# Performance work log

Hardware: AMD Instinct MI355X
Metric: run time of the kernel (lower is better)

Reference implementation:

```python
import jax, jax.numpy as jnp
import numpy as np

N = 10000        # nodes
E = 320000       # edges (before self-loops)
G = 100          # graphs in batch
HEADS = 2
OUT = 125        # per-head out channels
NEG_SLOPE = 0.2  # PyG GATConv default leaky_relu slope


def setup_inputs() -> dict:
    key = jax.random.key(0)
    k = lambda i: jax.random.fold_in(key, i)
    rn = lambda i, shape, s=0.1: jax.random.normal(k(i), shape, jnp.float32) * s
    inp = {
        "x": jax.random.normal(k(0), (N, 336), jnp.float32),
        "edge_index": jax.random.randint(k(1), (2, E), 0, N, jnp.int32),
        "batch": jnp.sort(jax.random.randint(k(2), (N,), 0, G, jnp.int32)),
    }
    conv_in = [336, 250, 250, 250]
    for i, din in enumerate(conv_in, start=1):
        base = 10 * i
        inp[f"W{i}"] = rn(base, (din, HEADS * OUT))
        inp[f"asrc{i}"] = rn(base + 1, (HEADS, OUT))
        inp[f"adst{i}"] = rn(base + 2, (HEADS, OUT))
        inp[f"b{i}"] = jnp.zeros((HEADS * OUT,), jnp.float32)
    lin_dims = [(250, 200), (200, 100), (100, 100), (100, 29)]
    for i, (din, dout) in enumerate(lin_dims, start=1):
        inp[f"lw{i}"] = rn(100 + i, (din, dout))
        inp[f"lb{i}"] = jnp.zeros((dout,), jnp.float32)
    return inp


def gat_conv(x, src, dst, W, asrc, adst, b):
    # PyG GATConv (v1), concat heads, self-loops already in (src, dst).
    n = x.shape[0]
    h = (x @ W).reshape(n, HEADS, OUT)                    # [N,H,C]
    e_src = jnp.einsum('nhc,hc->nh', h, asrc)             # a_src . h_j
    e_dst = jnp.einsum('nhc,hc->nh', h, adst)             # a_dst . h_i
    e = jax.nn.leaky_relu(e_src[src] + e_dst[dst], NEG_SLOPE)  # [Etot,H]
    m = jax.ops.segment_max(e, dst, num_segments=n)       # segment softmax over incoming edges
    e = jnp.exp(e - m[dst])
    denom = jax.ops.segment_sum(e, dst, num_segments=n)
    alpha = e / (denom[dst] + 1e-16)                      # [Etot,H]
    out = jax.ops.segment_sum(alpha[:, :, None] * h[src], dst, num_segments=n)
    return out.reshape(n, HEADS * OUT) + b


def reference(x, edge_index, batch,
              W1, asrc1, adst1, b1, W2, asrc2, adst2, b2,
              W3, asrc3, adst3, b3, W4, asrc4, adst4, b4,
              lw1, lb1, lw2, lb2, lw3, lb3, lw4, lb4):
    n = x.shape[0]
    loop = jnp.arange(n, dtype=edge_index.dtype)
    src = jnp.concatenate([edge_index[0], loop])          # add_self_loops=True
    dst = jnp.concatenate([edge_index[1], loop])

    h = jax.nn.relu(gat_conv(x, src, dst, W1, asrc1, adst1, b1))
    h = jax.nn.relu(gat_conv(h, src, dst, W2, asrc2, adst2, b2))
    h = jax.nn.relu(gat_conv(h, src, dst, W3, asrc3, adst3, b3))
    h = jax.nn.relu(gat_conv(h, src, dst, W4, asrc4, adst4, b4))

    # global_mean_pool over graph ids
    sums = jax.ops.segment_sum(h, batch, num_segments=G)
    cnts = jax.ops.segment_sum(jnp.ones((n, 1), h.dtype), batch, num_segments=G)
    g = sums / jnp.maximum(cnts, 1.0)                     # [G,250]

    g = jax.nn.relu(g @ lw1 + lb1)
    g = jax.nn.relu(g @ lw2 + lb2)
    g = jax.nn.relu(g @ lw3 + lb3)
    return g @ lw4 + lb4                                  # [G,29]
```

## Files before the change

kernel.cpp:

```cpp
#include <hip/hip_runtime.h>
#include <hip/hip_bf16.h>

#define NNODES 10000
#define NEDGES 320000
#define ETOT   (NEDGES + NNODES)
#define NGRAPH 100
#define CH     250
#define HOUT   125
#define MPAD   10048
#define NTILE  157
#define KP0    352
#define KP1    256
#define HPAD   256
#define ECAP   128
#define DCAPW  128
#define APAD   264

typedef __attribute__((ext_vector_type(8))) short bf16x8;
typedef __attribute__((ext_vector_type(4))) float f32x4;

static __device__ __forceinline__ float bflo(unsigned int u){
  union{ unsigned int i; float f; } v; v.i = u << 16; return v.f;
}
static __device__ __forceinline__ float bfhi(unsigned int u){
  union{ unsigned int i; float f; } v; v.i = u & 0xffff0000u; return v.f;
}
static __device__ __forceinline__ unsigned short f2bfbits(float f){
  __hip_bfloat16 b = __float2bfloat16(f);
  union{ __hip_bfloat16 b; unsigned short s; } v; v.b = b; return v.s;
}

struct Args {
  const float* x; const int* eidx; const int* batch;
  const float *W0,*W1,*W2,*W3;
  __hip_bfloat16 *Abf0, *Wt0, *Wt1, *Wt2, *Wt3;
  int *cursor; unsigned short* bucket; int *gstart;
};

__global__ void k_pre(Args a){
  int gtid = blockIdx.x * blockDim.x + threadIdx.x;
  int gstr = gridDim.x * blockDim.x;
  for (int e = gtid; e < ETOT; e += gstr){
    int dst, src;
    if (e < NEDGES){ src = a.eidx[e]; dst = a.eidx[NEDGES + e]; }
    else           { src = e - NEDGES; dst = src; }
    int pos = atomicAdd(&a.cursor[dst], 1);
    if (pos < ECAP) a.bucket[(size_t)dst * ECAP + pos] = (unsigned short)src;
  }
  for (int n = gtid; n < NNODES; n += gstr){
    int b1 = a.batch[n];
    int b0 = (n == 0) ? -1 : a.batch[n-1];
    for (int b = b0 + 1; b <= b1; ++b) a.gstart[b] = n;
    if (n == NNODES - 1){
      for (int b = b1 + 1; b <= NGRAPH; ++b) a.gstart[b] = NNODES;
    }
  }
  for (int j = gtid; j < NNODES * 84; j += gstr){
    int r = j / 84, c4 = (j - r * 84) * 4;
    float4 v = *(const float4*)(a.x + (size_t)r * 336 + c4);
    ushort4 o;
    o.x = f2bfbits(v.x); o.y = f2bfbits(v.y); o.z = f2bfbits(v.z); o.w = f2bfbits(v.w);
    *(ushort4*)(a.Abf0 + (size_t)r * KP0 + c4) = o;
  }
  const int T0 = 16 * KP0 * 16;
  const int T1 = 16 * KP1 * 16;
  int tot = T0 + 3*T1;
  for (int i = gtid; i < tot; i += gstr){
    const float* W; __hip_bfloat16* Wt; int K, Kp, li;
    if (i < T0)             { W = a.W0; Wt = a.Wt0; K = 336; Kp = KP0; li = i; }
    else if (i < T0 +   T1) { W = a.W1; Wt = a.Wt1; K = CH;  Kp = KP1; li = i - T0; }
    else if (i < T0 + 2*T1) { W = a.W2; Wt = a.Wt2; K = CH;  Kp = KP1; li = i - T0 - T1; }
    else                    { W = a.W3; Wt = a.Wt3; K = CH;  Kp = KP1; li = i - T0 - 2*T1; }
    int KC = Kp >> 5;
    int nt = li / (Kp * 16);
    int rem = li % (Kp * 16);
    int k = rem / 16;
    int n = rem % 16;
    int col = nt * 16 + n;
    float v = (k < K && col < CH) ? W[(size_t)k * CH + col] : 0.f;
    Wt[(((size_t)nt * KC + (k >> 5)) * 16 + n) * 32 + (k & 31)] = __float2bfloat16(v);
  }
}

__global__ __launch_bounds__(256) void k_gemm(
    const __hip_bfloat16* __restrict__ A, const __hip_bfloat16* __restrict__ Wt,
    __hip_bfloat16* __restrict__ Cb, const float* __restrict__ asrc,
    const float* __restrict__ adst, float* __restrict__ esrc, float* __restrict__ edst,
    int Kp){
  int wv = threadIdx.x >> 6, lane = threadIdx.x & 63;
  int n16 = lane & 15, q = lane >> 4;
  int KC = Kp >> 5;
  int rowbase = blockIdx.x * 64 + wv * 16;
  int bn = blockIdx.y * 64;
  int nt0 = bn >> 4;
  const __hip_bfloat16* ap = A  + (size_t)(rowbase + n16) * Kp + q * 8;
  const __hip_bfloat16* bp = Wt + ((size_t)nt0 * KC * 16 + n16) * 32 + q * 8;
  f32x4 ac0 = {0.f,0.f,0.f,0.f}, ac1 = ac0, ac2 = ac0, ac3 = ac0;
  for (int kc = 0; kc < KC; ++kc){
    bf16x8 a  = *(const bf16x8*)(ap + (size_t)kc * 32);
    bf16x8 b0 = *(const bf16x8*)(bp + ((size_t)0 * KC + kc) * 512);
    bf16x8 b1 = *(const bf16x8*)(bp + ((size_t)1 * KC + kc) * 512);
    bf16x8 b2 = *(const bf16x8*)(bp + ((size_t)2 * KC + kc) * 512);
    bf16x8 b3 = *(const bf16x8*)(bp + ((size_t)3 * KC + kc) * 512);
    ac0 = __builtin_amdgcn_mfma_f32_16x16x32_bf16(a, b0, ac0, 0, 0, 0);
    ac1 = __builtin_amdgcn_mfma_f32_16x16x32_bf16(a, b1, ac1, 0, 0, 0);
    ac2 = __builtin_amdgcn_mfma_f32_16x16x32_bf16(a, b2, ac2, 0, 0, 0);
    ac3 = __builtin_amdgcn_mfma_f32_16x16x32_bf16(a, b3, ac3, 0, 0, 0);
  }
  float es0[4] = {}, es1[4] = {}, ed0a[4] = {}, ed1a[4] = {};
  #define SCORE_T(AC, T) { \
    int col = bn + (T)*16 + n16; \
    bool ok = col < CH; \
    float av = ok ? asrc[col] : 0.f; \
    float dv = ok ? adst[col] : 0.f; \
    bool hh = col >= HOUT; \
    float av0 = hh ? 0.f : av, av1 = hh ? av : 0.f; \
    float dv0 = hh ? 0.f : dv, dv1 = hh ? dv : 0.f; \
    _Pragma("unroll") \
    for (int r = 0; r < 4; ++r){ \
      es0[r] += AC[r]*av0; es1[r] += AC[r]*av1; \
      ed0a[r] += AC[r]*dv0; ed1a[r] += AC[r]*dv1; } }
  SCORE_T(ac0, 0) SCORE_T(ac1, 1) SCORE_T(ac2, 2) SCORE_T(ac3, 3)
  #undef SCORE_T
  #pragma unroll
  for (int off = 1; off < 16; off <<= 1){
    #pragma unroll
    for (int r = 0; r < 4; ++r){
      es0[r]  += __shfl_xor(es0[r],  off);
      es1[r]  += __shfl_xor(es1[r],  off);
      ed0a[r] += __shfl_xor(ed0a[r], off);
      ed1a[r] += __shfl_xor(ed1a[r], off);
    }
  }
  if (n16 == 0){
    #pragma unroll
    for (int r = 0; r < 4; ++r){
      int row = rowbase + q*4 + r;
      if (row < NNODES){
        atomicAdd(&esrc[row*2+0], es0[r]);
        atomicAdd(&esrc[row*2+1], es1[r]);
        atomicAdd(&edst[row*2+0], ed0a[r]);
        atomicAdd(&edst[row*2+1], ed1a[r]);
      }
    }
  }
  #pragma unroll
  for (int r = 0; r < 4; ++r){
    int row = rowbase + q * 4 + r;
    if (row >= NNODES) continue;
    int col = bn + n16;
    __hip_bfloat16* cb = Cb + (size_t)row * HPAD + col;
    cb[0]  = __float2bfloat16(col      < CH ? ac0[r] : 0.f);
    cb[16] = __float2bfloat16(col + 16 < CH ? ac1[r] : 0.f);
    cb[32] = __float2bfloat16(col + 32 < CH ? ac2[r] : 0.f);
    cb[48] = __float2bfloat16(col + 48 < CH ? ac3[r] : 0.f);
  }
}

__global__ __launch_bounds__(1024, 8) void k_fused(
    const __hip_bfloat16* __restrict__ hcur,
    const float* __restrict__ esrc, const float* __restrict__ edst,
    const int* __restrict__ degv, const unsigned short* __restrict__ bucket,
    const float* __restrict__ bias,
    const __hip_bfloat16* __restrict__ Wt,
    const float* __restrict__ asrc, const float* __restrict__ adst,
    __hip_bfloat16* __restrict__ hnext,
    float* __restrict__ esN, float* __restrict__ edN){
  int w = threadIdx.x >> 6, lane = threadIdx.x & 63;
  int nodebase = blockIdx.x * 16;
  int node = nodebase + w;
  __shared__ unsigned short s_src[16][DCAPW];
  __shared__ float2 s_x[16][DCAPW];
  __shared__ short  h_lds[16][APAD];
  __shared__ float  esp[16][16][2];
  __shared__ float  edp[16][16][2];
  int deg = degv[node]; if (deg > ECAP) deg = ECAP;
  const unsigned short* __restrict__ eb = bucket + (size_t)node * ECAP;
  float ed0 = edst[node*2+0], ed1 = edst[node*2+1];
  float sm0 = 0.f, sm1 = 0.f;
  for (int i = lane; i < deg; i += 64){
    int src = eb[i];
    float2 ev = *(const float2*)(esrc + (size_t)src * 2);
    float e0 = ev.x + ed0; e0 = e0 > 0.f ? e0 : 0.2f*e0;
    float e1 = ev.y + ed1; e1 = e1 > 0.f ? e1 : 0.2f*e1;
    float x0 = __expf(e0), x1 = __expf(e1);
    s_src[w][i] = (unsigned short)src; s_x[w][i] = make_float2(x0, x1);
    sm0 += x0; sm1 += x1;
  }
  #pragma unroll
  for (int off = 32; off > 0; off >>= 1){
    sm0 += __shfl_xor(sm0, off);
    sm1 += __shfl_xor(sm1, off);
  }
  float inv0 = 1.f / (sm0 + 1e-16f);
  float inv1 = 1.f / (sm1 + 1e-16f);
  int half = lane >> 5, hl = lane & 31;
  int c0 = hl * 8;
  int n0 = HOUT - c0; n0 = n0 < 0 ? 0 : (n0 > 8 ? 8 : n0);
  const __hip_bfloat16* __restrict__ hrow = hcur + c0;
  float acc[8] = {0.f,0.f,0.f,0.f,0.f,0.f,0.f,0.f};
  #define EDGE(IDX) { \
    bool vld = (IDX) < deg; \
    int jj = vld ? (IDX) : 0; \
    int s = s_src[w][jj]; \
    float2 xv = s_x[w][jj]; \
    float a0 = vld ? xv.x : 0.f; \
    float a1 = vld ? xv.y : 0.f; \
    uint4 d = *(const uint4*)(hrow + (size_t)s * HPAD); \
    acc[0] += (0 < n0 ? a0 : a1) * bflo(d.x); \
    acc[1] += (1 < n0 ? a0 : a1) * bfhi(d.x); \
    acc[2] += (2 < n0 ? a0 : a1) * bflo(d.y); \
    acc[3] += (3 < n0 ? a0 : a1) * bfhi(d.y); \
    acc[4] += (4 < n0 ? a0 : a1) * bflo(d.z); \
    acc[5] += (5 < n0 ? a0 : a1) * bfhi(d.z); \
    acc[6] += (6 < n0 ? a0 : a1) * bflo(d.w); \
    acc[7] += (7 < n0 ? a0 : a1) * bfhi(d.w); }
  for (int it = half; it < deg; it += 8){
    EDGE(it)
    EDGE(it + 2)
    EDGE(it + 4)
    EDGE(it + 6)
  }
  #undef EDGE
  #pragma unroll
  for (int j = 0; j < 8; ++j) acc[j] += __shfl_xor(acc[j], 32);
  if (half == 0){
    if (hl < 31){
      float4 bA = *(const float4*)&bias[c0];
      float4 bB = *(const float4*)&bias[c0 + 4];
      float v0 = acc[0]*(0 < n0 ? inv0 : inv1) + bA.x;
      float v1 = acc[1]*(1 < n0 ? inv0 : inv1) + bA.y;
      float v2 = acc[2]*(2 < n0 ? inv0 : inv1) + bA.z;
      float v3 = acc[3]*(3 < n0 ? inv0 : inv1) + bA.w;
      float v4 = acc[4]*(4 < n0 ? inv0 : inv1) + bB.x;
      float v5 = acc[5]*(5 < n0 ? inv0 : inv1) + bB.y;
      float v6 = acc[6]*(6 < n0 ? inv0 : inv1) + bB.z;
      float v7 = acc[7]*(7 < n0 ? inv0 : inv1) + bB.w;
      v0 = v0 > 0.f ? v0 : 0.f; v1 = v1 > 0.f ? v1 : 0.f;
      v2 = v2 > 0.f ? v2 : 0.f; v3 = v3 > 0.f ? v3 : 0.f;
      v4 = v4 > 0.f ? v4 : 0.f; v5 = v5 > 0.f ? v5 : 0.f;
      v6 = v6 > 0.f ? v6 : 0.f; v7 = v7 > 0.f ? v7 : 0.f;
      uint4 o;
      o.x = (unsigned int)f2bfbits(v0) | ((unsigned int)f2bfbits(v1) << 16);
      o.y = (unsigned int)f2bfbits(v2) | ((unsigned int)f2bfbits(v3) << 16);
      o.z = (unsigned int)f2bfbits(v4) | ((unsigned int)f2bfbits(v5) << 16);
      o.w = (unsigned int)f2bfbits(v6) | ((unsigned int)f2bfbits(v7) << 16);
      *(uint4*)&h_lds[w][hl*8] = o;
    } else {
      float v0 = acc[0]*inv1 + bias[248];
      float v1 = acc[1]*inv1 + bias[249];
      v0 = v0 > 0.f ? v0 : 0.f; v1 = v1 > 0.f ? v1 : 0.f;
      uint4 o;
      o.x = (unsigned int)f2bfbits(v0) | ((unsigned int)f2bfbits(v1) << 16);
      o.y = 0u; o.z = 0u; o.w = 0u;
      *(uint4*)&h_lds[w][248] = o;
    }
  }
  __syncthreads();
  int n16 = lane & 15, q = lane >> 4;
  const int KC = KP1 >> 5;
  const __hip_bfloat16* bp = Wt + ((size_t)w * KC * 16 + n16) * 32 + q * 8;
  const short* ap = &h_lds[n16][q * 8];
  f32x4 ac = {0.f,0.f,0.f,0.f};
  #pragma unroll
  for (int kc = 0; kc < KC; ++kc){
    bf16x8 av = *(const bf16x8*)(ap + kc * 32);
    bf16x8 bv = *(const bf16x8*)(bp + (size_t)kc * 512);
    ac = __builtin_amdgcn_mfma_f32_16x16x32_bf16(av, bv, ac, 0, 0, 0);
  }
  int col = w * 16 + n16;
  bool ok = col < CH;
  float av_ = ok ? asrc[col] : 0.f;
  float dv_ = ok ? adst[col] : 0.f;
  bool hh = col >= HOUT;
  float av0 = hh ? 0.f : av_, av1 = hh ? av_ : 0.f;
  float dv0 = hh ? 0.f : dv_, dv1 = hh ? dv_ : 0.f;
  float es0[4], es1[4], edd0[4], edd1[4];
  #pragma unroll
  for (int r = 0; r < 4; ++r){
    es0[r] = ac[r]*av0; es1[r] = ac[r]*av1;
    edd0[r] = ac[r]*dv0; edd1[r] = ac[r]*dv1;
  }
  #pragma unroll
  for (int off = 1; off < 16; off <<= 1){
    #pragma unroll
    for (int r = 0; r < 4; ++r){
      es0[r]  += __shfl_xor(es0[r],  off);
      es1[r]  += __shfl_xor(es1[r],  off);
      edd0[r] += __shfl_xor(edd0[r], off);
      edd1[r] += __shfl_xor(edd1[r], off);
    }
  }
  if (n16 == 0){
    #pragma unroll
    for (int r = 0; r < 4; ++r){
      esp[w][q*4+r][0] = es0[r];  esp[w][q*4+r][1] = es1[r];
      edp[w][q*4+r][0] = edd0[r]; edp[w][q*4+r][1] = edd1[r];
    }
  }
  #pragma unroll
  for (int r = 0; r < 4; ++r){
    int row = nodebase + q*4 + r;
    hnext[(size_t)row * HPAD + col] = __float2bfloat16(ok ? ac[r] : 0.f);
  }
  __syncthreads();
  int t = threadIdx.x;
  if (t < 64){
    int row = t >> 2;
    int he = t & 1;
    int which = (t >> 1) & 1;
    float s = 0.f;
    #pragma unroll
    for (int w2 = 0; w2 < 16; ++w2)
      s += which ? edp[w2][row][he] : esp[w2][row][he];
    (which ? edN : esN)[(size_t)(nodebase + row) * 2 + he] = s;
  }
}

__global__ __launch_bounds__(256) void k_attn(const __hip_bfloat16* __restrict__ h,
                        const float* __restrict__ esrc, const float* __restrict__ edst,
                        const int* __restrict__ degv, const unsigned short* __restrict__ bucket,
                        const float* __restrict__ bias, __hip_bfloat16* __restrict__ outb){
  int wv = threadIdx.x >> 6, lane = threadIdx.x & 63;
  int node = blockIdx.x * 4 + wv;
  __shared__ unsigned short s_src[4][DCAPW];
  __shared__ float2 s_x[4][DCAPW];
  int deg = degv[node]; if (deg > ECAP) deg = ECAP;
  const unsigned short* __restrict__ eb = bucket + (size_t)node * ECAP;
  float ed0 = edst[node*2+0], ed1 = edst[node*2+1];
  float sm0 = 0.f, sm1 = 0.f;
  for (int i = lane; i < deg; i += 64){
    int src = eb[i];
    float2 ev = *(const float2*)(esrc + (size_t)src * 2);
    float e0 = ev.x + ed0; e0 = e0 > 0.f ? e0 : 0.2f*e0;
    float e1 = ev.y + ed1; e1 = e1 > 0.f ? e1 : 0.2f*e1;
    float x0 = __expf(e0), x1 = __expf(e1);
    s_src[wv][i] = (unsigned short)src; s_x[wv][i] = make_float2(x0, x1);
    sm0 += x0; sm1 += x1;
  }
  #pragma unroll
  for (int off = 32; off > 0; off >>= 1){
    sm0 += __shfl_xor(sm0, off);
    sm1 += __shfl_xor(sm1, off);
  }
  float inv0 = 1.f / (sm0 + 1e-16f);
  float inv1 = 1.f / (sm1 + 1e-16f);
  int half = lane >> 5, hl = lane & 31;
  int c0 = hl * 8;
  int n0 = HOUT - c0; n0 = n0 < 0 ? 0 : (n0 > 8 ? 8 : n0);
  const __hip_bfloat16* __restrict__ hrow = h + c0;
  float acc[8] = {0.f,0.f,0.f,0.f,0.f,0.f,0.f,0.f};
  #define EDGE(IDX) { \
    bool vld = (IDX) < deg; \
    int jj = vld ? (IDX) : 0; \
    int s = s_src[wv][jj]; \
    float2 xv = s_x[wv][jj]; \
    float a0 = vld ? xv.x : 0.f; \
    float a1 = vld ? xv.y : 0.f; \
    uint4 d = *(const uint4*)(hrow + (size_t)s * HPAD); \
    acc[0] += (0 < n0 ? a0 : a1) * bflo(d.x); \
    acc[1] += (1 < n0 ? a0 : a1) * bfhi(d.x); \
    acc[2] += (2 < n0 ? a0 : a1) * bflo(d.y); \
    acc[3] += (3 < n0 ? a0 : a1) * bfhi(d.y); \
    acc[4] += (4 < n0 ? a0 : a1) * bflo(d.z); \
    acc[5] += (5 < n0 ? a0 : a1) * bfhi(d.z); \
    acc[6] += (6 < n0 ? a0 : a1) * bflo(d.w); \
    acc[7] += (7 < n0 ? a0 : a1) * bfhi(d.w); }
  for (int it = half; it < deg; it += 8){
    EDGE(it)
    EDGE(it + 2)
    EDGE(it + 4)
    EDGE(it + 6)
  }
  #undef EDGE
  #pragma unroll
  for (int j = 0; j < 8; ++j) acc[j] += __shfl_xor(acc[j], 32);
  if (half == 0){
    if (hl < 31){
      float4 bA = *(const float4*)&bias[c0];
      float4 bB = *(const float4*)&bias[c0 + 4];
      float v0 = acc[0]*(0 < n0 ? inv0 : inv1) + bA.x;
      float v1 = acc[1]*(1 < n0 ? inv0 : inv1) + bA.y;
      float v2 = acc[2]*(2 < n0 ? inv0 : inv1) + bA.z;
      float v3 = acc[3]*(3 < n0 ? inv0 : inv1) + bA.w;
      float v4 = acc[4]*(4 < n0 ? inv0 : inv1) + bB.x;
      float v5 = acc[5]*(5 < n0 ? inv0 : inv1) + bB.y;
      float v6 = acc[6]*(6 < n0 ? inv0 : inv1) + bB.z;
      float v7 = acc[7]*(7 < n0 ? inv0 : inv1) + bB.w;
      v0 = v0 > 0.f ? v0 : 0.f; v1 = v1 > 0.f ? v1 : 0.f;
      v2 = v2 > 0.f ? v2 : 0.f; v3 = v3 > 0.f ? v3 : 0.f;
      v4 = v4 > 0.f ? v4 : 0.f; v5 = v5 > 0.f ? v5 : 0.f;
      v6 = v6 > 0.f ? v6 : 0.f; v7 = v7 > 0.f ? v7 : 0.f;
      uint4 o;
      o.x = (unsigned int)f2bfbits(v0) | ((unsigned int)f2bfbits(v1) << 16);
      o.y = (unsigned int)f2bfbits(v2) | ((unsigned int)f2bfbits(v3) << 16);
      o.z = (unsigned int)f2bfbits(v4) | ((unsigned int)f2bfbits(v5) << 16);
      o.w = (unsigned int)f2bfbits(v6) | ((unsigned int)f2bfbits(v7) << 16);
      *(uint4*)(outb + (size_t)node * KP1 + c0) = o;
    } else {
      float v0 = acc[0]*inv1 + bias[248];
      float v1 = acc[1]*inv1 + bias[249];
      v0 = v0 > 0.f ? v0 : 0.f; v1 = v1 > 0.f ? v1 : 0.f;
      unsigned int o = (unsigned int)f2bfbits(v0) | ((unsigned int)f2bfbits(v1) << 16);
      *(unsigned int*)(outb + (size_t)node * KP1 + 248) = o;
    }
  }
}

__global__ __launch_bounds__(256) void k_head(const __hip_bfloat16* __restrict__ xb,
                        const int* __restrict__ gstart,
                        const float* __restrict__ lw1, const float* __restrict__ lb1,
                        const float* __restrict__ lw2, const float* __restrict__ lb2,
                        const float* __restrict__ lw3, const float* __restrict__ lb3,
                        const float* __restrict__ lw4, const float* __restrict__ lb4,
                        float* __restrict__ out){
  int g = blockIdx.x;
  int tid = threadIdx.x;
  int s = gstart[g], e = gstart[g+1];
  __shared__ float gvec[256];
  __shared__ float m1[200];
  __shared__ float m2[112];
  __shared__ float m3[112];
  if (tid < 128){
    int c2 = tid * 2;
    const __hip_bfloat16* xp = xb + c2;
    float a0=0.f,a1=0.f,b0=0.f,b1=0.f;
    int n = s;
    for (; n + 3 < e; n += 4){
      unsigned int u0 = *(const unsigned int*)(xp + (size_t)n     * KP1);
      unsigned int u1 = *(const unsigned int*)(xp + (size_t)(n+1) * KP1);
      unsigned int u2 = *(const unsigned int*)(xp + (size_t)(n+2) * KP1);
      unsigned int u3 = *(const unsigned int*)(xp + (size_t)(n+3) * KP1);
      a0 += bflo(u0) + bflo(u2); a1 += bfhi(u0) + bfhi(u2);
      b0 += bflo(u1) + bflo(u3); b1 += bfhi(u1) + bfhi(u3);
    }
    for (; n < e; ++n){
      unsigned int u0 = *(const unsigned int*)(xp + (size_t)n * KP1);
      a0 += bflo(u0); a1 += bfhi(u0);
    }
    float scale = 1.f / fmaxf((float)(e - s), 1.f);
    gvec[c2]     = (a0 + b0) * scale;
    gvec[c2 + 1] = (a1 + b1) * scale;
  }
  __syncthreads();
  if (tid < 200){
    float a0=0.f,a1=0.f,a2=0.f,a3=0.f;
    int k = 0;
    for (; k + 3 < CH; k += 4){
      a0 += gvec[k]   * lw1[(size_t)k     * 200 + tid];
      a1 += gvec[k+1] * lw1[(size_t)(k+1) * 200 + tid];
      a2 += gvec[k+2] * lw1[(size_t)(k+2) * 200 + tid];
      a3 += gvec[k+3] * lw1[(size_t)(k+3) * 200 + tid];
    }
    for (; k < CH; ++k) a0 += gvec[k] * lw1[(size_t)k * 200 + tid];
    float v = a0 + a1 + a2 + a3 + lb1[tid];
    m1[tid] = v > 0.f ? v : 0.f;
  }
  __syncthreads();
  if (tid < 100){
    float a0=0.f,a1=0.f,a2=0.f,a3=0.f;
    for (int k = 0; k + 3 < 200; k += 4){
      a0 += m1[k]   * lw2[(size_t)k     * 100 + tid];
      a1 += m1[k+1] * lw2[(size_t)(k+1) * 100 + tid];
      a2 += m1[k+2] * lw2[(size_t)(k+2) * 100 + tid];
      a3 += m1[k+3] * lw2[(size_t)(k+3) * 100 + tid];
    }
    float v = a0 + a1 + a2 + a3 + lb2[tid];
    m2[tid] = v > 0.f ? v : 0.f;
  }
  __syncthreads();
  if (tid < 100){
    float a0=0.f,a1=0.f,a2=0.f,a3=0.f;
    for (int k = 0; k + 3 < 100; k += 4){
      a0 += m2[k]   * lw3[(size_t)k     * 100 + tid];
      a1 += m2[k+1] * lw3[(size_t)(k+1) * 100 + tid];
      a2 += m2[k+2] * lw3[(size_t)(k+2) * 100 + tid];
      a3 += m2[k+3] * lw3[(size_t)(k+3) * 100 + tid];
    }
    float v = a0 + a1 + a2 + a3 + lb3[tid];
    m3[tid] = v > 0.f ? v : 0.f;
  }
  __syncthreads();
  if (tid < 29){
    float a0=0.f,a1=0.f,a2=0.f,a3=0.f;
    for (int k = 0; k + 3 < 100; k += 4){
      a0 += m3[k]   * lw4[(size_t)k     * 29 + tid];
      a1 += m3[k+1] * lw4[(size_t)(k+1) * 29 + tid];
      a2 += m3[k+2] * lw4[(size_t)(k+2) * 29 + tid];
      a3 += m3[k+3] * lw4[(size_t)(k+3) * 29 + tid];
    }
    out[(size_t)g * 29 + tid] = a0 + a1 + a2 + a3 + lb4[tid];
  }
}

extern "C" void kernel_launch(void* const* d_in, const int* in_sizes, int n_in,
                              void* d_out, int out_size, void* d_ws, size_t ws_size,
                              hipStream_t stream){
  char* ws = (char*)d_ws;
  size_t off = 0;
  auto alloc = [&](size_t bytes)->void*{
    void* p = ws + off;
    off = (off + bytes + 255) & ~(size_t)255;
    return p;
  };
  __hip_bfloat16* hb16A = (__hip_bfloat16*)alloc((size_t)NNODES * HPAD * 2);
  __hip_bfloat16* hb16B = (__hip_bfloat16*)alloc((size_t)NNODES * HPAD * 2);
  __hip_bfloat16* Abf0 = (__hip_bfloat16*)alloc((size_t)MPAD * KP0 * 2);
  __hip_bfloat16* Abf  = (__hip_bfloat16*)alloc((size_t)MPAD * KP1 * 2);
  __hip_bfloat16* Wt0  = (__hip_bfloat16*)alloc((size_t)16 * KP0 * 16 * 2);
  __hip_bfloat16* Wt1  = (__hip_bfloat16*)alloc((size_t)16 * KP1 * 16 * 2);
  __hip_bfloat16* Wt2  = (__hip_bfloat16*)alloc((size_t)16 * KP1 * 16 * 2);
  __hip_bfloat16* Wt3  = (__hip_bfloat16*)alloc((size_t)16 * KP1 * 16 * 2);
  size_t zbeg = off;
  int*   cursor = (int*)  alloc((size_t)NNODES * 4);
  float* esA  = (float*)alloc((size_t)NNODES * 2 * 4);
  float* edA  = (float*)alloc((size_t)NNODES * 2 * 4);
  size_t zend = off;
  float* esB  = (float*)alloc((size_t)NNODES * 2 * 4);
  float* edB  = (float*)alloc((size_t)NNODES * 2 * 4);
  unsigned short* bucket = (unsigned short*)alloc((size_t)NNODES * ECAP * 2);
  int*   gstart = (int*)alloc((size_t)(NGRAPH + 1) * 4);

  hipMemsetAsync(ws + zbeg, 0, zend - zbeg, stream);

  Args a;
  a.x = (const float*)d_in[0];
  a.eidx = (const int*)d_in[1];
  a.batch = (const int*)d_in[2];
  a.W0 = (const float*)d_in[3];  a.W1 = (const float*)d_in[7];
  a.W2 = (const float*)d_in[11]; a.W3 = (const float*)d_in[15];
  a.Abf0 = Abf0;
  a.Wt0 = Wt0; a.Wt1 = Wt1; a.Wt2 = Wt2; a.Wt3 = Wt3;
  a.cursor = cursor; a.bucket = bucket; a.gstart = gstart;

  k_pre<<<(ETOT + 255)/256, 256, 0, stream>>>(a);

  k_gemm<<<dim3(NTILE, 4), 256, 0, stream>>>(Abf0, Wt0, hb16A,
      (const float*)d_in[4], (const float*)d_in[5], esA, edA, KP0);

  k_fused<<<NNODES/16, 1024, 0, stream>>>(hb16A, esA, edA, cursor, bucket,
      (const float*)d_in[6],  Wt1, (const float*)d_in[8],  (const float*)d_in[9],
      hb16B, esB, edB);
  k_fused<<<NNODES/16, 1024, 0, stream>>>(hb16B, esB, edB, cursor, bucket,
      (const float*)d_in[10], Wt2, (const float*)d_in[12], (const float*)d_in[13],
      hb16A, esA, edA);
  k_fused<<<NNODES/16, 1024, 0, stream>>>(hb16A, esA, edA, cursor, bucket,
      (const float*)d_in[14], Wt3, (const float*)d_in[16], (const float*)d_in[17],
      hb16B, esB, edB);

  k_attn<<<NNODES/4, 256, 0, stream>>>(hb16B, esB, edB, cursor, bucket,
      (const float*)d_in[18], Abf);

  k_head<<<NGRAPH, 256, 0, stream>>>(Abf, gstart,
      (const float*)d_in[19], (const float*)d_in[20],
      (const float*)d_in[21], (const float*)d_in[22],
      (const float*)d_in[23], (const float*)d_in[24],
      (const float*)d_in[25], (const float*)d_in[26],
      (float*)d_out);
}
```

Baseline: 293.3 us.

## Pad each attention head to 128 columns and aggregate heads in separate passes

Lays out the hidden features so head 0 sits in columns 0-124 and head 1 in columns 128-252. Weight transposes, score computation and the head's pooling read are remapped to match. The edge aggregation now uses 16 lanes per edge across 4 edges at a time, with one pass per head, so the per-lane head select disappears and each gather reads 256 contiguous bytes per head. The cost is twice as many passes over the edge list and extra shuffle reductions, in exchange for simpler inner-loop arithmetic and aligned writes.

Result: slower. 301.9 us (+2.9%).

```diff
diff --git a/kernel.cpp b/kernel.cpp
--- a/kernel.cpp
+++ b/kernel.cpp
@@ -19,6 +19,9 @@
 typedef __attribute__((ext_vector_type(8))) short bf16x8;
 typedef __attribute__((ext_vector_type(4))) float f32x4;
 
+#define OKC(c)  (((c) < HOUT) || ((c) >= 128 && (c) < 253))
+#define INVC(c) ((c) - ((c) >= 128 ? 3 : 0))
+
 static __device__ __forceinline__ float bflo(unsigned int u){
   union{ unsigned int i; float f; } v; v.i = u << 16; return v.f;
 }
@@ -28,6 +31,9 @@
 static __device__ __forceinline__ unsigned short f2bfbits(float f){
   __hip_bfloat16 b = __float2bfloat16(f);
   union{ __hip_bfloat16 b; unsigned short s; } v; v.b = b; return v.s;
+}
+static __device__ __forceinline__ unsigned int pk2(float lo, float hi){
+  return (unsigned int)f2bfbits(lo) | ((unsigned int)f2bfbits(hi) << 16);
 }
 
 struct Args {
@@ -66,18 +72,27 @@
   const int T1 = 16 * KP1 * 16;
   int tot = T0 + 3*T1;
   for (int i = gtid; i < tot; i += gstr){
-    const float* W; __hip_bfloat16* Wt; int K, Kp, li;
-    if (i < T0)             { W = a.W0; Wt = a.Wt0; K = 336; Kp = KP0; li = i; }
-    else if (i < T0 +   T1) { W = a.W1; Wt = a.Wt1; K = CH;  Kp = KP1; li = i - T0; }
-    else if (i < T0 + 2*T1) { W = a.W2; Wt = a.Wt2; K = CH;  Kp = KP1; li = i - T0 - T1; }
-    else                    { W = a.W3; Wt = a.Wt3; K = CH;  Kp = KP1; li = i - T0 - 2*T1; }
+    const float* W; __hip_bfloat16* Wt; int Kp, li, l0;
+    if (i < T0)             { W = a.W0; Wt = a.Wt0; Kp = KP0; li = i; l0 = 1; }
+    else if (i < T0 +   T1) { W = a.W1; Wt = a.Wt1; Kp = KP1; li = i - T0; l0 = 0; }
+    else if (i < T0 + 2*T1) { W = a.W2; Wt = a.Wt2; Kp = KP1; li = i - T0 - T1; l0 = 0; }
+    else                    { W = a.W3; Wt = a.Wt3; Kp = KP1; li = i - T0 - 2*T1; l0 = 0; }
     int KC = Kp >> 5;
     int nt = li / (Kp * 16);
     int rem = li % (Kp * 16);
     int k = rem / 16;
     int n = rem % 16;
-    int col = nt * 16 + n;
-    float v = (k < K && col < CH) ? W[(size_t)k * CH + col] : 0.f;
+    int nn = nt * 16 + n;
+    bool vc = OKC(nn);
+    int an = INVC(nn);
+    float v = 0.f;
+    if (l0){
+      if (k < 336 && vc) v = W[(size_t)k * CH + an];
+    } else {
+      bool vk = OKC(k);
+      int ak = INVC(k);
+      if (vk && vc) v = W[(size_t)ak * CH + an];
+    }
     Wt[(((size_t)nt * KC + (k >> 5)) * 16 + n) * 32 + (k & 31)] = __float2bfloat16(v);
   }
 }
@@ -110,10 +125,11 @@
   float es0[4] = {}, es1[4] = {}, ed0a[4] = {}, ed1a[4] = {};
   #define SCORE_T(AC, T) { \
     int col = bn + (T)*16 + n16; \
-    bool ok = col < CH; \
-    float av = ok ? asrc[col] : 0.f; \
-    float dv = ok ? adst[col] : 0.f; \
-    bool hh = col >= HOUT; \
+    bool ok = OKC(col); \
+    int act = INVC(col); \
+    float av = ok ? asrc[act] : 0.f; \
+    float dv = ok ? adst[act] : 0.f; \
+    bool hh = col >= 128; \
     float av0 = hh ? 0.f : av, av1 = hh ? av : 0.f; \
     float dv0 = hh ? 0.f : dv, dv1 = hh ? dv : 0.f; \
     _Pragma("unroll") \
@@ -150,12 +166,24 @@
     if (row >= NNODES) continue;
     int col = bn + n16;
     __hip_bfloat16* cb = Cb + (size_t)row * HPAD + col;
-    cb[0]  = __float2bfloat16(col      < CH ? ac0[r] : 0.f);
-    cb[16] = __float2bfloat16(col + 16 < CH ? ac1[r] : 0.f);
-    cb[32] = __float2bfloat16(col + 32 < CH ? ac2[r] : 0.f);
-    cb[48] = __float2bfloat16(col + 48 < CH ? ac3[r] : 0.f);
-  }
-}
+    cb[0]  = __float2bfloat16(OKC(col)      ? ac0[r] : 0.f);
+    cb[16] = __float2bfloat16(OKC(col + 16) ? ac1[r] : 0.f);
+    cb[32] = __float2bfloat16(OKC(col + 32) ? ac2[r] : 0.f);
+    cb[48] = __float2bfloat16(OKC(col + 48) ? ac3[r] : 0.f);
+  }
+}
+
+#define EDGEQ(IDX, ACC, HOFF, SEL, SS, SX) { \
+  int ii = (IDX) + quarter; \
+  bool vld = ii < deg; \
+  int jj = vld ? ii : 0; \
+  int s = SS[jj]; \
+  float aa = vld ? (SEL ? SX[jj].y : SX[jj].x) : 0.f; \
+  uint4 d = *(const uint4*)(hq + (size_t)s * HPAD + (HOFF)); \
+  ACC[0] += aa * bflo(d.x); ACC[1] += aa * bfhi(d.x); \
+  ACC[2] += aa * bflo(d.y); ACC[3] += aa * bfhi(d.y); \
+  ACC[4] += aa * bflo(d.z); ACC[5] += aa * bfhi(d.z); \
+  ACC[6] += aa * bflo(d.w); ACC[7] += aa * bfhi(d.w); }
 
 __global__ __launch_bounds__(1024, 8) void k_fused(
     const __hip_bfloat16* __restrict__ hcur,
@@ -194,67 +222,42 @@
   }
   float inv0 = 1.f / (sm0 + 1e-16f);
   float inv1 = 1.f / (sm1 + 1e-16f);
-  int half = lane >> 5, hl = lane & 31;
-  int c0 = hl * 8;
-  int n0 = HOUT - c0; n0 = n0 < 0 ? 0 : (n0 > 8 ? 8 : n0);
-  const __hip_bfloat16* __restrict__ hrow = hcur + c0;
-  float acc[8] = {0.f,0.f,0.f,0.f,0.f,0.f,0.f,0.f};
-  #define EDGE(IDX) { \
-    bool vld = (IDX) < deg; \
-    int jj = vld ? (IDX) : 0; \
-    int s = s_src[w][jj]; \
-    float2 xv = s_x[w][jj]; \
-    float a0 = vld ? xv.x : 0.f; \
-    float a1 = vld ? xv.y : 0.f; \
-    uint4 d = *(const uint4*)(hrow + (size_t)s * HPAD); \
-    acc[0] += (0 < n0 ? a0 : a1) * bflo(d.x); \
-    acc[1] += (1 < n0 ? a0 : a1) * bfhi(d.x); \
-    acc[2] += (2 < n0 ? a0 : a1) * bflo(d.y); \
-    acc[3] += (3 < n0 ? a0 : a1) * bfhi(d.y); \
-    acc[4] += (4 < n0 ? a0 : a1) * bflo(d.z); \
-    acc[5] += (5 < n0 ? a0 : a1) * bfhi(d.z); \
-    acc[6] += (6 < n0 ? a0 : a1) * bflo(d.w); \
-    acc[7] += (7 < n0 ? a0 : a1) * bfhi(d.w); }
-  for (int it = half; it < deg; it += 8){
-    EDGE(it)
-    EDGE(it + 2)
-    EDGE(it + 4)
-    EDGE(it + 6)
-  }
-  #undef EDGE
-  #pragma unroll
-  for (int j = 0; j < 8; ++j) acc[j] += __shfl_xor(acc[j], 32);
-  if (half == 0){
-    if (hl < 31){
-      float4 bA = *(const float4*)&bias[c0];
-      float4 bB = *(const float4*)&bias[c0 + 4];
-      float v0 = acc[0]*(0 < n0 ? inv0 : inv1) + bA.x;
-      float v1 = acc[1]*(1 < n0 ? inv0 : inv1) + bA.y;
-      float v2 = acc[2]*(2 < n0 ? inv0 : inv1) + bA.z;
-      float v3 = acc[3]*(3 < n0 ? inv0 : inv1) + bA.w;
-      float v4 = acc[4]*(4 < n0 ? inv0 : inv1) + bB.x;
-      float v5 = acc[5]*(5 < n0 ? inv0 : inv1) + bB.y;
-      float v6 = acc[6]*(6 < n0 ? inv0 : inv1) + bB.z;
-      float v7 = acc[7]*(7 < n0 ? inv0 : inv1) + bB.w;
-      v0 = v0 > 0.f ? v0 : 0.f; v1 = v1 > 0.f ? v1 : 0.f;
-      v2 = v2 > 0.f ? v2 : 0.f; v3 = v3 > 0.f ? v3 : 0.f;
-      v4 = v4 > 0.f ? v4 : 0.f; v5 = v5 > 0.f ? v5 : 0.f;
-      v6 = v6 > 0.f ? v6 : 0.f; v7 = v7 > 0.f ? v7 : 0.f;
-      uint4 o;
-      o.x = (unsigned int)f2bfbits(v0) | ((unsigned int)f2bfbits(v1) << 16);
-      o.y = (unsigned int)f2bfbits(v2) | ((unsigned int)f2bfbits(v3) << 16);
-      o.z = (unsigned int)f2bfbits(v4) | ((unsigned int)f2bfbits(v5) << 16);
-      o.w = (unsigned int)f2bfbits(v6) | ((unsigned int)f2bfbits(v7) << 16);
-      *(uint4*)&h_lds[w][hl*8] = o;
-    } else {
-      float v0 = acc[0]*inv1 + bias[248];
-      float v1 = acc[1]*inv1 + bias[249];
-      v0 = v0 > 0.f ? v0 : 0.f; v1 = v1 > 0.f ? v1 : 0.f;
-      uint4 o;
-      o.x = (unsigned int)f2bfbits(v0) | ((unsigned int)f2bfbits(v1) << 16);
-      o.y = 0u; o.z = 0u; o.w = 0u;
-      *(uint4*)&h_lds[w][248] = o;
-    }
+  int quarter = lane >> 4, ql = lane & 15;
+  const __hip_bfloat16* __restrict__ hq = hcur + ql * 8;
+  float a0c[8] = {0.f,0.f,0.f,0.f,0.f,0.f,0.f,0.f};
+  float a1c[8] = {0.f,0.f,0.f,0.f,0.f,0.f,0.f,0.f};
+  for (int it = 0; it < deg; it += 16){
+    EDGEQ(it,    a0c, 0, 0, s_src[w], s_x[w])
+    EDGEQ(it+4,  a0c, 0, 0, s_src[w], s_x[w])
+    EDGEQ(it+8,  a0c, 0, 0, s_src[w], s_x[w])
+    EDGEQ(it+12, a0c, 0, 0, s_src[w], s_x[w])
+  }
+  for (int it = 0; it < deg; it += 16){
+    EDGEQ(it,    a1c, 128, 1, s_src[w], s_x[w])
+    EDGEQ(it+4,  a1c, 128, 1, s_src[w], s_x[w])
+    EDGEQ(it+8,  a1c, 128, 1, s_src[w], s_x[w])
+    EDGEQ(it+12, a1c, 128, 1, s_src[w], s_x[w])
+  }
+  #pragma unroll
+  for (int j = 0; j < 8; ++j){
+    a0c[j] += __shfl_xor(a0c[j], 16); a0c[j] += __shfl_xor(a0c[j], 32);
+    a1c[j] += __shfl_xor(a1c[j], 16); a1c[j] += __shfl_xor(a1c[j], 32);
+  }
+  if (quarter < 2){
+    float invh = quarter ? inv1 : inv0;
+    const float* bh = bias + (quarter ? HOUT : 0);
+    float vals[8];
+    #pragma unroll
+    for (int j = 0; j < 8; ++j){
+      int c8 = ql*8 + j;
+      float t = (quarter ? a1c[j] : a0c[j]) * invh + ((c8 < HOUT) ? bh[c8] : 0.f);
+      t = t > 0.f ? t : 0.f;
+      vals[j] = (c8 < HOUT) ? t : 0.f;
+    }
+    uint4 o;
+    o.x = pk2(vals[0], vals[1]); o.y = pk2(vals[2], vals[3]);
+    o.z = pk2(vals[4], vals[5]); o.w = pk2(vals[6], vals[7]);
+    *(uint4*)&h_lds[w][(quarter ? 128 : 0) + ql*8] = o;
   }
   __syncthreads();
   int n16 = lane & 15, q = lane >> 4;
@@ -269,10 +272,11 @@
     ac = __builtin_amdgcn_mfma_f32_16x16x32_bf16(av, bv, ac, 0, 0, 0);
   }
   int col = w * 16 + n16;
-  bool ok = col < CH;
-  float av_ = ok ? asrc[col] : 0.f;
-  float dv_ = ok ? adst[col] : 0.f;
-  bool hh = col >= HOUT;
+  bool ok = OKC(col);
+  int act = INVC(col);
+  float av_ = ok ? asrc[act] : 0.f;
+  float dv_ = ok ? adst[act] : 0.f;
+  bool hh = col >= 128;
   float av0 = hh ? 0.f : av_, av1 = hh ? av_ : 0.f;
   float dv0 = hh ? 0.f : dv_, dv1 = hh ? dv_ : 0.f;
   float es0[4], es1[4], edd0[4], edd1[4];
@@ -345,65 +349,42 @@
   }
   float inv0 = 1.f / (sm0 + 1e-16f);
   float inv1 = 1.f / (sm1 + 1e-16f);
-  int half = lane >> 5, hl = lane & 31;
-  int c0 = hl * 8;
-  int n0 = HOUT - c0; n0 = n0 < 0 ? 0 : (n0 > 8 ? 8 : n0);
-  const __hip_bfloat16* __restrict__ hrow = h + c0;
-  float acc[8] = {0.f,0.f,0.f,0.f,0.f,0.f,0.f,0.f};
-  #define EDGE(IDX) { \
-    bool vld = (IDX) < deg; \
-    int jj = vld ? (IDX) : 0; \
-    int s = s_src[wv][jj]; \
-    float2 xv = s_x[wv][jj]; \
-    float a0 = vld ? xv.x : 0.f; \
-    float a1 = vld ? xv.y : 0.f; \
-    uint4 d = *(const uint4*)(hrow + (size_t)s * HPAD); \
-    acc[0] += (0 < n0 ? a0 : a1) * bflo(d.x); \
-    acc[1] += (1 < n0 ? a0 : a1) * bfhi(d.x); \
-    acc[2] += (2 < n0 ? a0 : a1) * bflo(d.y); \
-    acc[3] += (3 < n0 ? a0 : a1) * bfhi(d.y); \
-    acc[4] += (4 < n0 ? a0 : a1) * bflo(d.z); \
-    acc[5] += (5 < n0 ? a0 : a1) * bfhi(d.z); \
-    acc[6] += (6 < n0 ? a0 : a1) * bflo(d.w); \
-    acc[7] += (7 < n0 ? a0 : a1) * bfhi(d.w); }
-  for (int it = half; it < deg; it += 8){
-    EDGE(it)
-    EDGE(it + 2)
-    EDGE(it + 4)
-    EDGE(it + 6)
-  }
-  #undef EDGE
-  #pragma unroll
-  for (int j = 0; j < 8; ++j) acc[j] += __shfl_xor(acc[j], 32);
-  if (half == 0){
-    if (hl < 31){
-      float4 bA = *(const float4*)&bias[c0];
-      float4 bB = *(const float4*)&bias[c0 + 4];
-      float v0 = acc[0]*(0 < n0 ? inv0 : inv1) + bA.x;
-      float v1 = acc[1]*(1 < n0 ? inv0 : inv1) + bA.y;
-      float v2 = acc[2]*(2 < n0 ? inv0 : inv1) + bA.z;
-      float v3 = acc[3]*(3 < n0 ? inv0 : inv1) + bA.w;
-      float v4 = acc[4]*(4 < n0 ? inv0 : inv1) + bB.x;
-      float v5 = acc[5]*(5 < n0 ? inv0 : inv1) + bB.y;
-      float v6 = acc[6]*(6 < n0 ? inv0 : inv1) + bB.z;
-      float v7 = acc[7]*(7 < n0 ? inv0 : inv1) + bB.w;
-      v0 = v0 > 0.f ? v0 : 0.f; v1 = v1 > 0.f ? v1 : 0.f;
-      v2 = v2 > 0.f ? v2 : 0.f; v3 = v3 > 0.f ? v3 : 0.f;
-      v4 = v4 > 0.f ? v4 : 0.f; v5 = v5 > 0.f ? v5 : 0.f;
-      v6 = v6 > 0.f ? v6 : 0.f; v7 = v7 > 0.f ? v7 : 0.f;
-      uint4 o;
-      o.x = (unsigned int)f2bfbits(v0) | ((unsigned int)f2bfbits(v1) << 16);
-      o.y = (unsigned int)f2bfbits(v2) | ((unsigned int)f2bfbits(v3) << 16);
-      o.z = (unsigned int)f2bfbits(v4) | ((unsigned int)f2bfbits(v5) << 16);
-      o.w = (unsigned int)f2bfbits(v6) | ((unsigned int)f2bfbits(v7) << 16);
-      *(uint4*)(outb + (size_t)node * KP1 + c0) = o;
-    } else {
-      float v0 = acc[0]*inv1 + bias[248];
-      float v1 = acc[1]*inv1 + bias[249];
-      v0 = v0 > 0.f ? v0 : 0.f; v1 = v1 > 0.f ? v1 : 0.f;
-      unsigned int o = (unsigned int)f2bfbits(v0) | ((unsigned int)f2bfbits(v1) << 16);
-      *(unsigned int*)(outb + (size_t)node * KP1 + 248) = o;
-    }
+  int quarter = lane >> 4, ql = lane & 15;
+  const __hip_bfloat16* __restrict__ hq = h + ql * 8;
+  float a0c[8] = {0.f,0.f,0.f,0.f,0.f,0.f,0.f,0.f};
+  float a1c[8] = {0.f,0.f,0.f,0.f,0.f,0.f,0.f,0.f};
+  for (int it = 0; it < deg; it += 16){
+    EDGEQ(it,    a0c, 0, 0, s_src[wv], s_x[wv])
+    EDGEQ(it+4,  a0c, 0, 0, s_src[wv], s_x[wv])
+    EDGEQ(it+8,  a0c, 0, 0, s_src[wv], s_x[wv])
+    EDGEQ(it+12, a0c, 0, 0, s_src[wv], s_x[wv])
+  }
+  for (int it = 0; it < deg; it += 16){
+    EDGEQ(it,    a1c, 128, 1, s_src[wv], s_x[wv])
+    EDGEQ(it+4,  a1c, 128, 1, s_src[wv], s_x[wv])
+    EDGEQ(it+8,  a1c, 128, 1, s_src[wv], s_x[wv])
+    EDGEQ(it+12, a1c, 128, 1, s_src[wv], s_x[wv])
+  }
+  #pragma unroll
+  for (int j = 0; j < 8; ++j){
+    a0c[j] += __shfl_xor(a0c[j], 16); a0c[j] += __shfl_xor(a0c[j], 32);
+    a1c[j] += __shfl_xor(a1c[j], 16); a1c[j] += __shfl_xor(a1c[j], 32);
+  }
+  if (quarter < 2){
+    float invh = quarter ? inv1 : inv0;
+    const float* bh = bias + (quarter ? HOUT : 0);
+    float vals[8];
+    #pragma unroll
+    for (int j = 0; j < 8; ++j){
+      int c8 = ql*8 + j;
+      float t = (quarter ? a1c[j] : a0c[j]) * invh + ((c8 < HOUT) ? bh[c8] : 0.f);
+      t = t > 0.f ? t : 0.f;
+      vals[j] = (c8 < HOUT) ? t : 0.f;
+    }
+    uint4 o;
+    o.x = pk2(vals[0], vals[1]); o.y = pk2(vals[2], vals[3]);
+    o.z = pk2(vals[4], vals[5]); o.w = pk2(vals[6], vals[7]);
+    *(uint4*)(outb + (size_t)node * KP1 + (quarter ? 128 : 0) + ql*8) = o;
   }
 }
 
@@ -418,6 +399,7 @@
   int tid = threadIdx.x;
   int s = gstart[g], e = gstart[g+1];
   __shared__ float gvec[256];
+  __shared__ float cvec[256];
   __shared__ float m1[200];
   __shared__ float m2[112];
   __shared__ float m3[112];
@@ -443,16 +425,18 @@
     gvec[c2 + 1] = (a1 + b1) * scale;
   }
   __syncthreads();
+  if (tid < CH) cvec[tid] = gvec[tid + (tid >= HOUT ? 3 : 0)];
+  __syncthreads();
   if (tid < 200){
     float a0=0.f,a1=0.f,a2=0.f,a3=0.f;
     int k = 0;
     for (; k + 3 < CH; k += 4){
-      a0 += gvec[k]   * lw1[(size_t)k     * 200 + tid];
-      a1 += gvec[k+1] * lw1[(size_t)(k+1) * 200 + tid];
-      a2 += gvec[k+2] * lw1[(size_t)(k+2) * 200 + tid];
-      a3 += gvec[k+3] * lw1[(size_t)(k+3) * 200 + tid];
-    }
-    for (; k < CH; ++k) a0 += gvec[k] * lw1[(size_t)k * 200 + tid];
+      a0 += cvec[k]   * lw1[(size_t)k     * 200 + tid];
+      a1 += cvec[k+1] * lw1[(size_t)(k+1) * 200 + tid];
+      a2 += cvec[k+2] * lw1[(size_t)(k+2) * 200 + tid];
+      a3 += cvec[k+3] * lw1[(size_t)(k+3) * 200 + tid];
+    }
+    for (; k < CH; ++k) a0 += cvec[k] * lw1[(size_t)k * 200 + tid];
     float v = a0 + a1 + a2 + a3 + lb1[tid];
     m1[tid] = v > 0.f ? v : 0.f;
   }
```
